# Optimization experiments

Hardware: AMD Instinct MI355X
Metric: run time of the kernel (lower is better)

The kernel has to match this reference:

```python
import jax, jax.numpy as jnp
import numpy as np

B, C, H, W = 512, 1, 280, 280
K, S, F = 28, 28, 10           # kernel, stride, nfilters
HS, WS = 10, 10                # output spatial spans (280/28)
SPAN = HS * WS                 # 100 patch locations
OUT = 10                       # out_channels
DEC_IN = HS * WS * F           # 1000


def setup_inputs() -> dict:
    key = jax.random.key(0)
    k1, k2, k3, k4, k5 = jax.random.split(key, 5)
    x = jax.random.normal(k1, (B, C, H, W), dtype=jnp.float32)
    # locally-connected weights: one kernel per (filter, spatial location), torch layout [F*SPAN, C, K, K]
    conv_w = jax.random.normal(k2, (F * SPAN, C, K, K), dtype=jnp.float32) * 0.02
    conv_b = jax.random.normal(k3, (F * SPAN, C), dtype=jnp.float32) * 0.02
    dec_w = jax.random.normal(k4, (OUT, DEC_IN), dtype=jnp.float32) * 0.02
    dec_b = jax.random.normal(k5, (OUT,), dtype=jnp.float32) * 0.02
    return {"x": x, "conv_w": conv_w, "conv_b": conv_b, "dec_w": dec_w, "dec_b": dec_b}


def reference(x, conv_w, conv_b, dec_w, dec_b):
    # Extract non-overlapping KxK patches (stride == kernel_size, padding == 0):
    # [B,C,H,W] -> [B,C,HS,K,WS,K] -> [B,HS,WS,C,K,K] -> [B,SPAN,C,K,K]
    # matches torch unfold(2).unfold(3) ordering (height span outer, width span inner).
    patches = x.reshape(B, C, HS, K, WS, K).transpose(0, 2, 4, 1, 3, 5)
    patches = patches.reshape(B, SPAN, C, K, K)
    # weight index in torch is f*SPAN + s (x is tiled SPAN-fastest by repeat)
    w = conv_w.reshape(F, SPAN, C, K, K)
    # per-location elementwise mul + reduce over (kh, kw) == batched tiny contraction
    out = jnp.einsum('bscij,fscij->bfsc', patches, w)  # [B,F,SPAN,C]
    out = out + conv_b.reshape(F, SPAN, C)
    out = out.reshape(B, F, HS, WS)  # valid since C == 1 (as in torch view)
    out = jax.nn.relu(out).reshape(B, DEC_IN)
    return out @ dec_w.T + dec_b
```

## Files before the change

kernel.cpp:

```cpp
#include <hip/hip_runtime.h>
#include <hip/hip_bf16.h>

#define HW      280
#define IMG     78400
#define KK      28
#define F_N     10
#define SPAN    100
#define OUT_N   10
#define P_PLANE 512000

typedef short s16x8 __attribute__((ext_vector_type(8)));
typedef float f32x4 __attribute__((ext_vector_type(4)));

static __device__ __forceinline__ unsigned bits2(__hip_bfloat162 h) {
  return *reinterpret_cast<unsigned*>(&h);
}

#define RAW_BARRIER() asm volatile("s_waitcnt lgkmcnt(0)\ns_barrier" ::: "memory")

__global__ __launch_bounds__(256) void wprep(const float* __restrict__ cw,
                                             uint4* __restrict__ wbuf4) {
  const int idx = blockIdx.x * 256 + (int)threadIdx.x;
  const int k8  = idx & 3;
  const int f   = (idx >> 2) & 15;
  const int rs  = idx >> 6;
  const int r   = rs % 28;
  const int s   = rs / 28;
  uint4 out = make_uint4(0, 0, 0, 0);
  if (f < F_N) {
    const float* base = cw + (size_t)(f * SPAN + s) * (KK * KK) + r * KK + k8 * 8;
    const float4 a = *reinterpret_cast<const float4*>(base);
    out.x = bits2(__float22bfloat162_rn(make_float2(a.x, a.y)));
    out.y = bits2(__float22bfloat162_rn(make_float2(a.z, a.w)));
    if (k8 < 3) {
      const float4 c = *reinterpret_cast<const float4*>(base + 4);
      out.z = bits2(__float22bfloat162_rn(make_float2(c.x, c.y)));
      out.w = bits2(__float22bfloat162_rn(make_float2(c.z, c.w)));
    }
  }
  wbuf4[idx] = out;
}

__global__ __launch_bounds__(256, 4) void lcn_conv(
    const float* __restrict__ x, const unsigned short* __restrict__ wbuf,
    float* __restrict__ P) {
  const int bid  = blockIdx.x;
  const int xcd  = bid & 7;
  const int grp  = bid >> 3;
  const int hsrq = xcd + 8 * (grp % 5);
  const int bg   = grp / 5;
  const int hs   = hsrq >> 2;
  const int rq   = hsrq & 3;

  const int tid  = (int)threadIdx.x;
  const int lane = tid & 63;
  const int wid  = tid >> 6;
  const int l15  = lane & 15;
  const int kg   = lane >> 4;

  __shared__ short xl[2][16 * 320];

  for (int i = tid; i < 2 * 160; i += 256) {
    const int buf = i / 160, j = i - buf * 160;
    const int b = j / 10, ws = j - b * 10;
    const int sidx = (b * 320 + ws * 32 + 28) ^ ((b & 7) << 3);
    *reinterpret_cast<short4*>(&xl[buf][sidx]) = make_short4(0, 0, 0, 0);
  }

  const int nun = (wid < 2) ? 3 : 2;
  const int wsl[3] = {wid, wid + 4, wid + 8};

  f32x4 acc[3];
#pragma unroll
  for (int u = 0; u < 3; ++u) acc[u] = (f32x4){0.f, 0.f, 0.f, 0.f};

  const int row0 = hs * KK + rq * 7;
  const float* xbase = x + (size_t)bg * 16 * IMG + (size_t)row0 * HW;

  float4 stgA[5], stgB[5];

#define ISSUE(STG, R)                                                       \
  _Pragma("unroll")                                                         \
  for (int j = 0; j < 5; ++j) {                                             \
    const int i = tid + 256 * j;                                            \
    if (i < 1120) {                                                         \
      const int b = i / 70, q = i - b * 70;                                 \
      STG[j] = *reinterpret_cast<const float4*>(                            \
          xbase + (size_t)b * IMG + (size_t)(R) * HW + q * 4);              \
    }                                                                       \
  }

#define COMMIT(STG, BUF)                                                    \
  _Pragma("unroll")                                                         \
  for (int j = 0; j < 5; ++j) {                                             \
    const int i = tid + 256 * j;                                            \
    if (i < 1120) {                                                         \
      const int b = i / 70, q = i - b * 70;                                 \
      const int ws = q / 7, c4 = q - ws * 7;                                \
      const int sidx = (b * 320 + ws * 32 + c4 * 4) ^ ((b & 7) << 3);       \
      uint2 pk;                                                             \
      pk.x = bits2(__float22bfloat162_rn(make_float2(STG[j].x, STG[j].y))); \
      pk.y = bits2(__float22bfloat162_rn(make_float2(STG[j].z, STG[j].w))); \
      *reinterpret_cast<uint2*>(&xl[BUF][sidx]) = pk;                       \
    }                                                                       \
  }

  ISSUE(stgA, 0)
  ISSUE(stgB, 1)
  COMMIT(stgA, 0)
  RAW_BARRIER();

#pragma unroll
  for (int r = 0; r < 7; ++r) {
    const int buf = r & 1;
    const int rr  = rq * 7 + r;

    s16x8 bfr[3];
#pragma unroll
    for (int u = 0; u < 3; ++u)
      bfr[u] = *reinterpret_cast<const s16x8*>(
          wbuf + (size_t)((hs * 10 + wsl[u]) * 28 + rr) * 512 + l15 * 32 + kg * 8);

    if (r + 2 < 7) {
      if (r & 1) { ISSUE(stgB, r + 2) } else { ISSUE(stgA, r + 2) }
    }

#pragma unroll
    for (int u = 0; u < 3; ++u) {
      if (u < nun) {
        const int ws = wsl[u];
        const int sidx = (l15 * 320 + ws * 32 + kg * 8) ^ ((l15 & 7) << 3);
        const s16x8 afr = *reinterpret_cast<const s16x8*>(&xl[buf][sidx]);
        acc[u] = __builtin_amdgcn_mfma_f32_16x16x32_bf16(afr, bfr[u], acc[u], 0, 0, 0);
      }
    }

    if (r < 6) {
      if (r & 1) { COMMIT(stgA, buf ^ 1) } else { COMMIT(stgB, buf ^ 1) }
      RAW_BARRIER();
    }
  }

  if (l15 < F_N) {
#pragma unroll
    for (int u = 0; u < 3; ++u) {
      if (u < nun) {
        const int s = hs * 10 + wsl[u];
        float* Pp = P + (size_t)rq * P_PLANE + (size_t)(l15 * SPAN + s) * 512
                      + bg * 16 + kg * 4;
        *reinterpret_cast<float4*>(Pp) =
            make_float4(acc[u][0], acc[u][1], acc[u][2], acc[u][3]);
      }
    }
  }
}

__global__ __launch_bounds__(512) void lcn_dec(
    const float* __restrict__ P, const float* __restrict__ cb,
    const float* __restrict__ dw, float* __restrict__ yp) {
  const int dchunk = blockIdx.x;
  const int b      = (int)threadIdx.x;

  const float* Pb = P + b;
  float acc[OUT_N];
#pragma unroll
  for (int o = 0; o < OUT_N; ++o) acc[o] = 0.f;

#pragma unroll
  for (int dd = 0; dd < 20; ++dd) {
    const int d = dchunk * 20 + dd;
    const float* pd = Pb + (size_t)d * 512;
    const float p = pd[0] + pd[P_PLANE] + pd[2 * (size_t)P_PLANE]
                          + pd[3 * (size_t)P_PLANE];
    const float h = fmaxf(p + cb[d], 0.f);
#pragma unroll
    for (int o = 0; o < OUT_N; ++o)
      acc[o] = fmaf(h, dw[o * 1000 + d], acc[o]);
  }
#pragma unroll
  for (int o = 0; o < OUT_N; ++o)
    yp[(size_t)(dchunk * OUT_N + o) * 512 + b] = acc[o];
}

__global__ __launch_bounds__(128) void lcn_yred(
    const float* __restrict__ yp, const float* __restrict__ db,
    float* __restrict__ y) {
  const int idx = blockIdx.x * 128 + (int)threadIdx.x;
  const int o = idx >> 9;
  const int b = idx & 511;
  float a = db[o];
#pragma unroll 10
  for (int p = 0; p < 50; ++p) a += yp[(size_t)p * 5120 + idx];
  y[b * OUT_N + o] = a;
}

extern "C" void kernel_launch(void* const* d_in, const int* in_sizes, int n_in,
                              void* d_out, int out_size, void* d_ws, size_t ws_size,
                              hipStream_t stream) {
  const float* x  = (const float*)d_in[0];
  const float* cw = (const float*)d_in[1];
  const float* cb = (const float*)d_in[2];
  const float* dw = (const float*)d_in[3];
  const float* db = (const float*)d_in[4];
  float* y = (float*)d_out;

  float*    P    = (float*)d_ws;
  float*    yp   = P + 4 * (size_t)P_PLANE;
  uint4*    wbuf = (uint4*)(yp + 50 * 5120);

  wprep   <<<dim3(700),  dim3(256), 0, stream>>>(cw, wbuf);
  lcn_conv<<<dim3(1280), dim3(256), 0, stream>>>(x, (const unsigned short*)wbuf, P);
  lcn_dec <<<dim3(50),   dim3(512), 0, stream>>>(P, cb, dw, yp);
  lcn_yred<<<dim3(40),   dim3(128), 0, stream>>>(yp, db, y);
}
```

Before: 45.34 us.

## Rework weight prep to one thread per row and split decoder reduction across waves

The weight-prep kernel now assigns one thread per 28-wide weight row and writes the padded 16-filter bf16 layout directly, dropping the launch from 700 to 110 blocks and removing the work of padding threads. The decoder now runs 200 blocks of 256 threads, each wave covering 10 d values for 64 batch elements, and combines the four waves through shared memory. This halves the number of partial sums (25 instead of 50) that the final reduction kernel reads. The aim is more parallelism in the small tail kernels, at the cost of a block barrier and some shared-memory traffic.

```diff
diff --git a/kernel.cpp b/kernel.cpp
--- a/kernel.cpp
+++ b/kernel.cpp
@@ -21,24 +21,30 @@
 __global__ __launch_bounds__(256) void wprep(const float* __restrict__ cw,
                                              uint4* __restrict__ wbuf4) {
   const int idx = blockIdx.x * 256 + (int)threadIdx.x;
-  const int k8  = idx & 3;
-  const int f   = (idx >> 2) & 15;
-  const int rs  = idx >> 6;
-  const int r   = rs % 28;
-  const int s   = rs / 28;
-  uint4 out = make_uint4(0, 0, 0, 0);
-  if (f < F_N) {
-    const float* base = cw + (size_t)(f * SPAN + s) * (KK * KK) + r * KK + k8 * 8;
-    const float4 a = *reinterpret_cast<const float4*>(base);
-    out.x = bits2(__float22bfloat162_rn(make_float2(a.x, a.y)));
-    out.y = bits2(__float22bfloat162_rn(make_float2(a.z, a.w)));
-    if (k8 < 3) {
-      const float4 c = *reinterpret_cast<const float4*>(base + 4);
-      out.z = bits2(__float22bfloat162_rn(make_float2(c.x, c.y)));
-      out.w = bits2(__float22bfloat162_rn(make_float2(c.z, c.w)));
-    }
-  }
-  wbuf4[idx] = out;
+  if (idx >= 28000) return;
+  const int fs = idx / 28;
+  const int r  = idx - fs * 28;
+  const int f  = fs / 100;
+  const int s  = fs - f * 100;
+
+  const float* src = cw + (size_t)idx * 28;
+  float v[28];
+#pragma unroll
+  for (int j = 0; j < 7; ++j)
+    *reinterpret_cast<float4*>(&v[j * 4]) =
+        *reinterpret_cast<const float4*>(src + j * 4);
+
+  unsigned p[16];
+#pragma unroll
+  for (int k2 = 0; k2 < 14; ++k2)
+    p[k2] = bits2(__float22bfloat162_rn(make_float2(v[2 * k2], v[2 * k2 + 1])));
+  p[14] = 0u; p[15] = 0u;
+
+  uint4* dst = wbuf4 + ((size_t)(s * 28 + r) * 16 + f) * 4;
+  dst[0] = make_uint4(p[0],  p[1],  p[2],  p[3]);
+  dst[1] = make_uint4(p[4],  p[5],  p[6],  p[7]);
+  dst[2] = make_uint4(p[8],  p[9],  p[10], p[11]);
+  dst[3] = make_uint4(p[12], p[13], p[14], p[15]);
 }
 
 __global__ __launch_bounds__(256, 4) void lcn_conv(
@@ -155,11 +161,15 @@
   }
 }
 
-__global__ __launch_bounds__(512) void lcn_dec(
+__global__ __launch_bounds__(256) void lcn_dec(
     const float* __restrict__ P, const float* __restrict__ cb,
     const float* __restrict__ dw, float* __restrict__ yp) {
-  const int dchunk = blockIdx.x;
-  const int b      = (int)threadIdx.x;
+  const int dchunk = blockIdx.x >> 3;
+  const int bgrp   = blockIdx.x & 7;
+  const int tid    = (int)threadIdx.x;
+  const int bl     = tid & 63;
+  const int dway   = tid >> 6;
+  const int b      = bgrp * 64 + bl;
 
   const float* Pb = P + b;
   float acc[OUT_N];
@@ -167,8 +177,8 @@
   for (int o = 0; o < OUT_N; ++o) acc[o] = 0.f;
 
 #pragma unroll
-  for (int dd = 0; dd < 20; ++dd) {
-    const int d = dchunk * 20 + dd;
+  for (int dd = 0; dd < 10; ++dd) {
+    const int d = dchunk * 40 + dway * 10 + dd;
     const float* pd = Pb + (size_t)d * 512;
     const float p = pd[0] + pd[P_PLANE] + pd[2 * (size_t)P_PLANE]
                           + pd[3 * (size_t)P_PLANE];
@@ -177,20 +187,31 @@
     for (int o = 0; o < OUT_N; ++o)
       acc[o] = fmaf(h, dw[o * 1000 + d], acc[o]);
   }
-#pragma unroll
-  for (int o = 0; o < OUT_N; ++o)
-    yp[(size_t)(dchunk * OUT_N + o) * 512 + b] = acc[o];
-}
-
-__global__ __launch_bounds__(128) void lcn_yred(
+
+  __shared__ float red[3][OUT_N][64];
+  if (dway > 0) {
+#pragma unroll
+    for (int o = 0; o < OUT_N; ++o) red[dway - 1][o][bl] = acc[o];
+  }
+  __syncthreads();
+  if (dway == 0) {
+#pragma unroll
+    for (int o = 0; o < OUT_N; ++o) {
+      const float v = acc[o] + red[0][o][bl] + red[1][o][bl] + red[2][o][bl];
+      yp[(size_t)(dchunk * OUT_N + o) * 512 + b] = v;
+    }
+  }
+}
+
+__global__ __launch_bounds__(256) void lcn_yred(
     const float* __restrict__ yp, const float* __restrict__ db,
     float* __restrict__ y) {
-  const int idx = blockIdx.x * 128 + (int)threadIdx.x;
+  const int idx = blockIdx.x * 256 + (int)threadIdx.x;
   const int o = idx >> 9;
   const int b = idx & 511;
   float a = db[o];
-#pragma unroll 10
-  for (int p = 0; p < 50; ++p) a += yp[(size_t)p * 5120 + idx];
+#pragma unroll
+  for (int p = 0; p < 25; ++p) a += yp[(size_t)p * 5120 + idx];
   y[b * OUT_N + o] = a;
 }
 
@@ -204,12 +225,12 @@
   const float* db = (const float*)d_in[4];
   float* y = (float*)d_out;
 
-  float*    P    = (float*)d_ws;
-  float*    yp   = P + 4 * (size_t)P_PLANE;
-  uint4*    wbuf = (uint4*)(yp + 50 * 5120);
-
-  wprep   <<<dim3(700),  dim3(256), 0, stream>>>(cw, wbuf);
+  float* P  = (float*)d_ws;
+  float* yp = P + 4 * (size_t)P_PLANE;
+  uint4* wbuf = (uint4*)(yp + 25 * 5120);
+
+  wprep   <<<dim3(110),  dim3(256), 0, stream>>>(cw, wbuf);
   lcn_conv<<<dim3(1280), dim3(256), 0, stream>>>(x, (const unsigned short*)wbuf, P);
-  lcn_dec <<<dim3(50),   dim3(512), 0, stream>>>(P, cb, dw, yp);
-  lcn_yred<<<dim3(40),   dim3(128), 0, stream>>>(yp, db, y);
-}
+  lcn_dec <<<dim3(200),  dim3(256), 0, stream>>>(P, cb, dw, yp);
+  lcn_yred<<<dim3(20),   dim3(256), 0, stream>>>(yp, db, y);
+}
```

Measured after the change: 43.53 us. -4.0%, faster.

## Fuse weight bf16 conversion into conv and merge decoder reduction kernels

Applied to the files above, without the earlier changes.

Removes the separate weight-prep kernel: the conv kernel now loads fp32 weights straight from the original layout and converts them to bf16 fragments in registers, with rows outside the valid range clamped and padding lanes discarded at store. The decoder and final reduction kernels are merged into one kernel that stages the decoder weights and conv bias in shared memory, splits the 1000-wide reduction across 32 thread groups, and reduces them in shared memory before adding the output bias. This drops two kernel launches and the intermediate partial-sum buffer. In exchange the conv kernel does scattered, uncoalesced fp32 weight loads plus the conversion work, and the decoder now runs on only 32 blocks.

```diff
diff --git a/kernel.cpp b/kernel.cpp
--- a/kernel.cpp
+++ b/kernel.cpp
@@ -18,31 +18,8 @@
 
 #define RAW_BARRIER() asm volatile("s_waitcnt lgkmcnt(0)\ns_barrier" ::: "memory")
 
-__global__ __launch_bounds__(256) void wprep(const float* __restrict__ cw,
-                                             uint4* __restrict__ wbuf4) {
-  const int idx = blockIdx.x * 256 + (int)threadIdx.x;
-  const int k8  = idx & 3;
-  const int f   = (idx >> 2) & 15;
-  const int rs  = idx >> 6;
-  const int r   = rs % 28;
-  const int s   = rs / 28;
-  uint4 out = make_uint4(0, 0, 0, 0);
-  if (f < F_N) {
-    const float* base = cw + (size_t)(f * SPAN + s) * (KK * KK) + r * KK + k8 * 8;
-    const float4 a = *reinterpret_cast<const float4*>(base);
-    out.x = bits2(__float22bfloat162_rn(make_float2(a.x, a.y)));
-    out.y = bits2(__float22bfloat162_rn(make_float2(a.z, a.w)));
-    if (k8 < 3) {
-      const float4 c = *reinterpret_cast<const float4*>(base + 4);
-      out.z = bits2(__float22bfloat162_rn(make_float2(c.x, c.y)));
-      out.w = bits2(__float22bfloat162_rn(make_float2(c.z, c.w)));
-    }
-  }
-  wbuf4[idx] = out;
-}
-
 __global__ __launch_bounds__(256, 4) void lcn_conv(
-    const float* __restrict__ x, const unsigned short* __restrict__ wbuf,
+    const float* __restrict__ x, const float* __restrict__ cw,
     float* __restrict__ P) {
   const int bid  = blockIdx.x;
   const int xcd  = bid & 7;
@@ -69,6 +46,15 @@
 
   const int nun = (wid < 2) ? 3 : 2;
   const int wsl[3] = {wid, wid + 4, wid + 8};
+
+  const int fC = (l15 < F_N) ? l15 : 0;
+  const float* wrow[3];
+#pragma unroll
+  for (int u = 0; u < 3; ++u) {
+    const int sC = (wsl[u] < 10) ? (hs * 10 + wsl[u]) : (hs * 10);
+    wrow[u] = cw + (size_t)(fC * SPAN + sC) * (KK * KK) + kg * 8;
+  }
+  const int kOff2 = (kg == 3) ? 0 : 4;
 
   f32x4 acc[3];
 #pragma unroll
@@ -105,6 +91,20 @@
     }                                                                       \
   }
 
+#define BLOAD(BFR, RR)                                                      \
+  _Pragma("unroll")                                                         \
+  for (int u = 0; u < 3; ++u) {                                             \
+    const float* wp = wrow[u] + (RR) * KK;                                  \
+    const float4 w0 = *reinterpret_cast<const float4*>(wp);                 \
+    const float4 w1 = *reinterpret_cast<const float4*>(wp + kOff2);         \
+    union { unsigned q[4]; s16x8 v; } pk_;                                  \
+    pk_.q[0] = bits2(__float22bfloat162_rn(make_float2(w0.x, w0.y)));       \
+    pk_.q[1] = bits2(__float22bfloat162_rn(make_float2(w0.z, w0.w)));       \
+    pk_.q[2] = bits2(__float22bfloat162_rn(make_float2(w1.x, w1.y)));       \
+    pk_.q[3] = bits2(__float22bfloat162_rn(make_float2(w1.z, w1.w)));       \
+    BFR[u] = pk_.v;                                                         \
+  }
+
   ISSUE(stgA, 0)
   ISSUE(stgB, 1)
   COMMIT(stgA, 0)
@@ -116,10 +116,7 @@
     const int rr  = rq * 7 + r;
 
     s16x8 bfr[3];
-#pragma unroll
-    for (int u = 0; u < 3; ++u)
-      bfr[u] = *reinterpret_cast<const s16x8*>(
-          wbuf + (size_t)((hs * 10 + wsl[u]) * 28 + rr) * 512 + l15 * 32 + kg * 8);
+    BLOAD(bfr, rr)
 
     if (r + 2 < 7) {
       if (r & 1) { ISSUE(stgB, r + 2) } else { ISSUE(stgA, r + 2) }
@@ -155,43 +152,51 @@
   }
 }
 
-__global__ __launch_bounds__(512) void lcn_dec(
+__global__ __launch_bounds__(512) void lcn_dec2(
     const float* __restrict__ P, const float* __restrict__ cb,
-    const float* __restrict__ dw, float* __restrict__ yp) {
-  const int dchunk = blockIdx.x;
-  const int b      = (int)threadIdx.x;
-
-  const float* Pb = P + b;
+    const float* __restrict__ dw, const float* __restrict__ db,
+    float* __restrict__ y) {
+  const int tid  = (int)threadIdx.x;
+  const int b16  = tid & 15;
+  const int dway = tid >> 4;
+  const int b    = blockIdx.x * 16 + b16;
+
+  __shared__ float dwl[OUT_N * 1000];
+  __shared__ float cbl[1000];
+  for (int i = tid; i < OUT_N * 1000; i += 512) dwl[i] = dw[i];
+  for (int i = tid; i < 1000; i += 512) cbl[i] = cb[i];
+  __syncthreads();
+
   float acc[OUT_N];
 #pragma unroll
   for (int o = 0; o < OUT_N; ++o) acc[o] = 0.f;
 
-#pragma unroll
-  for (int dd = 0; dd < 20; ++dd) {
-    const int d = dchunk * 20 + dd;
-    const float* pd = Pb + (size_t)d * 512;
-    const float p = pd[0] + pd[P_PLANE] + pd[2 * (size_t)P_PLANE]
-                          + pd[3 * (size_t)P_PLANE];
-    const float h = fmaxf(p + cb[d], 0.f);
-#pragma unroll
-    for (int o = 0; o < OUT_N; ++o)
-      acc[o] = fmaf(h, dw[o * 1000 + d], acc[o]);
-  }
-#pragma unroll
-  for (int o = 0; o < OUT_N; ++o)
-    yp[(size_t)(dchunk * OUT_N + o) * 512 + b] = acc[o];
-}
-
-__global__ __launch_bounds__(128) void lcn_yred(
-    const float* __restrict__ yp, const float* __restrict__ db,
-    float* __restrict__ y) {
-  const int idx = blockIdx.x * 128 + (int)threadIdx.x;
-  const int o = idx >> 9;
-  const int b = idx & 511;
-  float a = db[o];
-#pragma unroll 10
-  for (int p = 0; p < 50; ++p) a += yp[(size_t)p * 5120 + idx];
-  y[b * OUT_N + o] = a;
+#pragma unroll 4
+  for (int k = 0; k < 32; ++k) {
+    const int d = dway + 32 * k;
+    if (d < 1000) {
+      const float* pd = P + (size_t)d * 512 + b;
+      const float p = pd[0] + pd[P_PLANE] + pd[2 * (size_t)P_PLANE]
+                            + pd[3 * (size_t)P_PLANE];
+      const float h = fmaxf(p + cbl[d], 0.f);
+#pragma unroll
+      for (int o = 0; o < OUT_N; ++o)
+        acc[o] = fmaf(h, dwl[o * 1000 + d], acc[o]);
+    }
+  }
+
+  __shared__ float red[32][OUT_N][16];
+#pragma unroll
+  for (int o = 0; o < OUT_N; ++o) red[dway][o][b16] = acc[o];
+  __syncthreads();
+
+  if (tid < 16 * OUT_N) {
+    const int bb = tid & 15, o = tid >> 4;
+    float a = db[o];
+#pragma unroll
+    for (int w2 = 0; w2 < 32; ++w2) a += red[w2][o][bb];
+    y[(blockIdx.x * 16 + bb) * OUT_N + o] = a;
+  }
 }
 
 extern "C" void kernel_launch(void* const* d_in, const int* in_sizes, int n_in,
@@ -204,12 +209,8 @@
   const float* db = (const float*)d_in[4];
   float* y = (float*)d_out;
 
-  float*    P    = (float*)d_ws;
-  float*    yp   = P + 4 * (size_t)P_PLANE;
-  uint4*    wbuf = (uint4*)(yp + 50 * 5120);
-
-  wprep   <<<dim3(700),  dim3(256), 0, stream>>>(cw, wbuf);
-  lcn_conv<<<dim3(1280), dim3(256), 0, stream>>>(x, (const unsigned short*)wbuf, P);
-  lcn_dec <<<dim3(50),   dim3(512), 0, stream>>>(P, cb, dw, yp);
-  lcn_yred<<<dim3(40),   dim3(128), 0, stream>>>(yp, db, y);
-}
+  float* P = (float*)d_ws;
+
+  lcn_conv<<<dim3(1280), dim3(256), 0, stream>>>(x, cw, P);
+  lcn_dec2<<<dim3(32),   dim3(512), 0, stream>>>(P, cb, dw, db, y);
+}
```

New measurement: 52.41 us. +15.6%, slower.
